# Kernel optimization log

Measured on AMD Instinct MI355X. Metric: run time of the kernel, lower is better.

## Reference

```python
import jax, jax.numpy as jnp
import numpy as np

EPS = 1e-5

def _lc(x, w, b, stride, pad):
    # x: [B,H,W]; w: [Ho,Wo,kh,kw]; b: [Ho,Wo]
    Ho, Wo, kh, kw = w.shape
    patches = jax.lax.conv_general_dilated_patches(
        x[:, None], (kh, kw), (stride, stride), [(pad, pad), (pad, pad)])
    # patches: [B, kh*kw, Ho, Wo]
    out = jnp.einsum('bkij,ijk->bij', patches, w.reshape(Ho, Wo, kh * kw))
    return out + b

def _ln2d(x, g, b):
    # torch LayerNorm over the last two (spatial) dims
    mu = x.mean(axis=(1, 2), keepdims=True)
    var = ((x - mu) ** 2).mean(axis=(1, 2), keepdims=True)
    return (x - mu) * jax.lax.rsqrt(var + EPS) * g + b

def _pool(x):
    # MaxPool2d(kernel=2, stride=2) over spatial dims of [B,H,W]
    return jax.lax.reduce_window(x, -jnp.inf, jax.lax.max, (1, 2, 2), (1, 2, 2), 'VALID')

def setup_inputs() -> dict:
    key = jax.random.key(0)
    ks = jax.random.split(key, 32)
    d = {}
    d['x'] = jax.random.normal(ks[0], (64, 128, 128), jnp.float32)
    sizes = [(128, 7), (64, 5), (64, 5), (32, 3), (32, 3), (16, 3)]
    for i, (s, k) in enumerate(sizes, start=1):
        d[f'w{i}'] = jax.random.normal(ks[4 * i], (s, s, k, k), jnp.float32) / k
        d[f'b{i}'] = jax.random.normal(ks[4 * i + 1], (s, s), jnp.float32)
        d[f'g{i}'] = jnp.ones((s, s), jnp.float32)
        d[f'be{i}'] = jnp.zeros((s, s), jnp.float32)
    d['fcw'] = jax.random.normal(ks[30], (1024, 256), jnp.float32) / np.sqrt(256.0)
    d['fcb'] = jax.random.normal(ks[31], (1024,), jnp.float32) * 0.01
    return d

def reference(x, w1, b1, g1, be1, w2, b2, g2, be2, w3, b3, g3, be3,
              w4, b4, g4, be4, w5, b5, g5, be5, w6, b6, g6, be6, fcw, fcb):
    # dropout is identity (eval / p=0)
    h = _pool(_ln2d(jax.nn.relu(_lc(x, w1, b1, 1, 3)), g1, be1))   # [B,64,64]
    h = _ln2d(jax.nn.relu(_lc(h, w2, b2, 1, 2)), g2, be2)          # [B,64,64]
    h = _pool(_ln2d(jax.nn.relu(_lc(h, w3, b3, 1, 2)), g3, be3))   # [B,32,32]
    h = _ln2d(jax.nn.relu(_lc(h, w4, b4, 1, 1)), g4, be4)          # [B,32,32]
    h = _pool(_ln2d(jax.nn.relu(_lc(h, w5, b5, 1, 1)), g5, be5))   # [B,16,16]
    h = _ln2d(jax.nn.relu(_lc(h, w6, b6, 1, 1)), g6, be6)          # [B,16,16]
    h = h.reshape(h.shape[0], -1) @ fcw.T + fcb                    # [B,1024]
    return jax.nn.softmax(h, axis=-1)
```

## Files before the change

### kernel.cpp

```cpp
#include <hip/hip_runtime.h>

#define LN_EPS 1e-5f

constexpr int T1_OFF   = 0;
constexpr int WT2_OFF  = 1048576;
constexpr int WT3_OFF  = WT2_OFF + 102400;
constexpr int WT4_OFF  = WT3_OFF + 102400;
constexpr int WT5_OFF  = WT4_OFF + 9216;
constexpr int WT6_OFF  = WT5_OFF + 9216;
constexpr int FCWT_OFF = WT6_OFF + 2304;
constexpr int R2_OFF   = FCWT_OFF + 262144;
constexpr int R3_OFF   = R2_OFF + 262144;
constexpr int R4_OFF   = R3_OFF + 262144;
constexpr int R5_OFF   = R4_OFF + 65536;
constexpr int ST1_OFF  = R5_OFF + 65536;
constexpr int ST2_OFF  = ST1_OFF + 32768;
constexpr int ST3_OFF  = ST2_OFF + 1024;
constexpr int ST4_OFF  = ST3_OFF + 1024;
constexpr int ST5_OFF  = ST4_OFF + 512;

constexpr int NREP = 136;

__global__ __launch_bounds__(256) void s1_conv(const float* __restrict__ x,
                                               const float* __restrict__ w1,
                                               const float* __restrict__ b1,
                                               const float* __restrict__ w2,
                                               const float* __restrict__ w3,
                                               const float* __restrict__ w4,
                                               const float* __restrict__ w5,
                                               const float* __restrict__ w6,
                                               const float* __restrict__ fcw,
                                               float* __restrict__ ws)
{
    const int tid = threadIdx.x;

    if (blockIdx.x < NREP) {
        const int rb = blockIdx.x;
        if (rb < 32) {
            for (int idx = rb * 256 + tid; idx < 102400; idx += 32 * 256) {
                int p = idx / 25, k = idx % 25;
                ws[WT2_OFF + k * 4096 + p] = w2[idx];
            }
        } else if (rb < 64) {
            for (int idx = (rb - 32) * 256 + tid; idx < 102400; idx += 32 * 256) {
                int p = idx / 25, k = idx % 25;
                ws[WT3_OFF + k * 4096 + p] = w3[idx];
            }
        } else if (rb < 68) {
            for (int idx = (rb - 64) * 256 + tid; idx < 9216; idx += 4 * 256) {
                int p = idx / 9, k = idx % 9;
                ws[WT4_OFF + k * 1024 + p] = w4[idx];
            }
        } else if (rb < 72) {
            for (int idx = (rb - 68) * 256 + tid; idx < 9216; idx += 4 * 256) {
                int p = idx / 9, k = idx % 9;
                ws[WT5_OFF + k * 1024 + p] = w5[idx];
            }
        } else if (rb < 73) {
            for (int idx = tid; idx < 2304; idx += 256) {
                int p = idx / 9, k = idx % 9;
                ws[WT6_OFF + k * 256 + p] = w6[idx];
            }
        } else {
            for (int idx = (rb - 73) * 256 + tid; idx < 262144; idx += 63 * 256) {
                int r = idx >> 8, kc = idx & 255;
                int kq = kc >> 2, c = kc & 3;
                ws[FCWT_OFF + kq * 4096 + r * 4 + c] = fcw[idx];
            }
        }
        return;
    }

    constexpr int R = 128, K = 7, TILE = 8, S = 16, PAD = 3;
    constexpr int RT = TILE + K - 1;
    constexpr int PP = RT * RT + 1;
    constexpr int NBLK = R / TILE;
    constexpr int WCNT = TILE * TILE * K * K;
    constexpr int PG = 256 / S;
    constexpr int OPT = TILE * TILE / PG;

    __shared__ float s_in[S * PP];
    __shared__ float s_w[WCNT];
    __shared__ float s_b[TILE * TILE];
    __shared__ float sp[4][16], sq[4][16];

    float* t1 = ws + T1_OFF;
    const int cb = blockIdx.x - NREP;
    const int bt = cb % (NBLK * NBLK);
    const int sg = cb / (NBLK * NBLK);
    const int i0 = (bt / NBLK) * TILE;
    const int j0 = (bt % NBLK) * TILE;
    const int S0 = sg * S;

    for (int idx = tid; idx < WCNT; idx += 256) {
        int pi = idx / (K * K), kk = idx % (K * K);
        int gi = i0 + pi / TILE, gj = j0 + pi % TILE;
        s_w[idx] = w1[(gi * R + gj) * (K * K) + kk];
    }
    if (tid < TILE * TILE)
        s_b[tid] = b1[(i0 + tid / TILE) * R + (j0 + tid % TILE)];

    for (int idx = tid; idx < S * RT * RT; idx += 256) {
        int ls = idx / (RT * RT), p = idx % (RT * RT);
        int ci = i0 - PAD + p / RT, cj = j0 - PAD + p % RT;
        float v = 0.0f;
        if (ci >= 0 && ci < R && cj >= 0 && cj < R)
            v = x[(S0 + ls) * R * R + ci * R + cj];
        s_in[ls * PP + p] = v;
    }
    __syncthreads();

    const int s = tid % S;
    const int pg = tid / S;
    const int p0 = pg * OPT;
    const int ti = p0 / TILE, tj0 = p0 % TILE;
    float acc[OPT];
    #pragma unroll
    for (int o = 0; o < OPT; o++) acc[o] = s_b[p0 + o];
    #pragma unroll
    for (int ki = 0; ki < K; ki++) {
        float row[OPT + K - 1];
        #pragma unroll
        for (int c = 0; c < OPT + K - 1; c++)
            row[c] = s_in[s * PP + (ti + ki) * RT + tj0 + c];
        #pragma unroll
        for (int kj = 0; kj < K; kj++)
            #pragma unroll
            for (int o = 0; o < OPT; o++)
                acc[o] += row[o + kj] * s_w[(p0 + o) * (K * K) + ki * K + kj];
    }
    float lsum = 0.f, lsq = 0.f;
    #pragma unroll
    for (int o = 0; o < OPT; o++) {
        float v = fmaxf(acc[o], 0.0f);
        t1[(S0 + s) * R * R + (i0 + ti) * R + (j0 + tj0 + o)] = v;
        lsum += v; lsq += v * v;
    }
    lsum += __shfl_xor(lsum, 16, 64); lsum += __shfl_xor(lsum, 32, 64);
    lsq  += __shfl_xor(lsq,  16, 64); lsq  += __shfl_xor(lsq,  32, 64);
    const int w = tid >> 6, l = tid & 63;
    if (l < 16) { sp[w][l] = lsum; sq[w][l] = lsq; }
    __syncthreads();
    if (tid < 16) {
        float a = sp[0][tid] + sp[1][tid] + sp[2][tid] + sp[3][tid];
        float b = sq[0][tid] + sq[1][tid] + sq[2][tid] + sq[3][tid];
        ws[ST1_OFF + (S0 + tid) * 512 + bt * 2]     = a;
        ws[ST1_OFF + (S0 + tid) * 512 + bt * 2 + 1] = b;
    }
}

__device__ __forceinline__ void block_sum2_256(float a, float b, float* red)
{
    const int tid = threadIdx.x;
    #pragma unroll
    for (int off = 32; off > 0; off >>= 1) {
        a += __shfl_down(a, off, 64);
        b += __shfl_down(b, off, 64);
    }
    if ((tid & 63) == 0) { red[tid >> 6] = a; red[4 + (tid >> 6)] = b; }
    __syncthreads();
    if (tid == 0) {
        red[0] = red[0] + red[1] + red[2] + red[3];
        red[4] = red[4] + red[5] + red[6] + red[7];
    }
    __syncthreads();
}

template<int M, int K, bool POOL>
__global__ __launch_bounds__(256) void stage_conv(
    const float* __restrict__ wsr, float* __restrict__ wsw,
    const float* __restrict__ g, const float* __restrict__ be,
    const float* __restrict__ bias,
    int inOff, int wtOff, int outOff,
    int stInOff, int nStatIn, float invNIn, int stOutOff)
{
    constexpr int NSLAB  = M / 8;
    constexpr int PADK   = (K - 1) / 2;
    constexpr int HR     = 8 + 2 * PADK;
    constexpr int IN_RES = POOL ? 2 * M : M;
    constexpr int STR    = M + 1;

    __shared__ float Isl[HR * STR];
    __shared__ float red[8];

    const int tid  = threadIdx.x;
    const int s    = blockIdx.x / NSLAB;
    const int slab = blockIdx.x % NSLAB;
    const int r0   = slab * 8;

    float a = 0.f, b = 0.f;
    for (int t = tid; t < nStatIn; t += 256) {
        a += wsr[stInOff + (s * nStatIn + t) * 2];
        b += wsr[stInOff + (s * nStatIn + t) * 2 + 1];
    }
    block_sum2_256(a, b, red);
    const float mu = red[0] * invNIn;
    const float rs = rsqrtf(red[4] * invNIn - mu * mu + LN_EPS);

    const float* In = wsr + inOff + s * (IN_RES * IN_RES);

    for (int idx = tid; idx < HR * M; idx += 256) {
        int lr = idx / M, jc = idx % M;
        int gr = r0 - PADK + lr;
        float v = 0.f;
        if (gr >= 0 && gr < M) {
            if constexpr (POOL) {
                float2 xa = *(const float2*)(In + (2 * gr) * IN_RES + 2 * jc);
                float2 xb = *(const float2*)(In + (2 * gr + 1) * IN_RES + 2 * jc);
                float2 ga = *(const float2*)(g  + (2 * gr) * IN_RES + 2 * jc);
                float2 gb = *(const float2*)(g  + (2 * gr + 1) * IN_RES + 2 * jc);
                float2 ea = *(const float2*)(be + (2 * gr) * IN_RES + 2 * jc);
                float2 eb = *(const float2*)(be + (2 * gr + 1) * IN_RES + 2 * jc);
                float n0 = (xa.x - mu) * rs * ga.x + ea.x;
                float n1 = (xa.y - mu) * rs * ga.y + ea.y;
                float n2 = (xb.x - mu) * rs * gb.x + eb.x;
                float n3 = (xb.y - mu) * rs * gb.y + eb.y;
                v = fmaxf(fmaxf(n0, n1), fmaxf(n2, n3));
            } else {
                int q = gr * M + jc;
                v = (In[q] - mu) * rs * g[q] + be[q];
            }
        }
        Isl[lr * STR + jc] = v;
    }
    __syncthreads();

    const float* wT = wsr + wtOff;
    constexpr int OPW = (8 * M) / 256;
    float lsum = 0.f, lsq = 0.f;
    #pragma unroll
    for (int o = 0; o < OPW; o++) {
        int p  = tid + o * 256;
        int li = p / M, j = p % M;
        int gi = r0 + li;
        int gp = gi * M + j;
        float acc = bias[gp];
        #pragma unroll
        for (int ki = 0; ki < K; ki++)
            #pragma unroll
            for (int kj = 0; kj < K; kj++) {
                int jj = j - PADK + kj;
                float iv = (jj >= 0 && jj < M) ? Isl[(li + ki) * STR + jj] : 0.f;
                acc += iv * wT[(ki * K + kj) * (M * M) + gp];
            }
        float v = fmaxf(acc, 0.f);
        wsw[outOff + s * (M * M) + gp] = v;
        lsum += v; lsq += v * v;
    }
    __syncthreads();
    block_sum2_256(lsum, lsq, red);
    if (tid == 0) {
        wsw[stOutOff + (s * NSLAB + slab) * 2]     = red[0];
        wsw[stOutOff + (s * NSLAB + slab) * 2 + 1] = red[4];
    }
}

constexpr int NT = 1024;
constexpr int NW = NT / 64;

__device__ __forceinline__ void stats_reduce(float* red, float lsum, float lsq,
                                             float inv_n, float* s_mu, float* s_rs)
{
    const int tid = threadIdx.x;
    #pragma unroll
    for (int off = 32; off > 0; off >>= 1) {
        lsum += __shfl_down(lsum, off, 64);
        lsq  += __shfl_down(lsq,  off, 64);
    }
    if ((tid & 63) == 0) { red[tid >> 6] = lsum; red[NW + (tid >> 6)] = lsq; }
    __syncthreads();
    if (tid == 0) {
        float a = 0.f, b = 0.f;
        #pragma unroll
        for (int i = 0; i < NW; i++) { a += red[i]; b += red[NW + i]; }
        float mu = a * inv_n, ms = b * inv_n;
        *s_mu = mu;
        *s_rs = rsqrtf(ms - mu * mu + LN_EPS);
    }
    __syncthreads();
}

__global__ __launch_bounds__(1024) void s6_tail(
    const float* __restrict__ wsr,
    const float* __restrict__ g5, const float* __restrict__ be5,
    const float* __restrict__ b6,
    const float* __restrict__ g6, const float* __restrict__ be6,
    const float* __restrict__ fcb,
    float* __restrict__ outp)
{
    __shared__ float I6[16 * 17];
    __shared__ float h[256];
    __shared__ float red[2 * NW];
    __shared__ float s_mu, s_rs;

    const int s = blockIdx.x;
    const int tid = threadIdx.x;

    if (tid == 0) {
        float a = 0.f, b = 0.f;
        #pragma unroll
        for (int i = 0; i < 4; i++) {
            a += wsr[ST5_OFF + (s * 4 + i) * 2];
            b += wsr[ST5_OFF + (s * 4 + i) * 2 + 1];
        }
        float mu = a * (1.f / 1024.f);
        s_mu = mu;
        s_rs = rsqrtf(b * (1.f / 1024.f) - mu * mu + LN_EPS);
    }
    __syncthreads();
    const float mu5 = s_mu, rs5 = s_rs;
    const float* R5 = wsr + R5_OFF + s * 1024;

    if (tid < 256) {
        int i = tid >> 4, j = tid & 15;
        float2 xa = *(const float2*)(R5 + (2 * i) * 32 + 2 * j);
        float2 xb = *(const float2*)(R5 + (2 * i + 1) * 32 + 2 * j);
        float2 ga = *(const float2*)(g5 + (2 * i) * 32 + 2 * j);
        float2 gb = *(const float2*)(g5 + (2 * i + 1) * 32 + 2 * j);
        float2 ea = *(const float2*)(be5 + (2 * i) * 32 + 2 * j);
        float2 eb = *(const float2*)(be5 + (2 * i + 1) * 32 + 2 * j);
        float n0 = (xa.x - mu5) * rs5 * ga.x + ea.x;
        float n1 = (xa.y - mu5) * rs5 * ga.y + ea.y;
        float n2 = (xb.x - mu5) * rs5 * gb.x + eb.x;
        float n3 = (xb.y - mu5) * rs5 * gb.y + eb.y;
        I6[i * 17 + j] = fmaxf(fmaxf(n0, n1), fmaxf(n2, n3));
    }
    __syncthreads();

    float v = 0.f, ls = 0.f, lq = 0.f;
    if (tid < 256) {
        int i = tid >> 4, j = tid & 15;
        const float* wT6 = wsr + WT6_OFF;
        float acc = b6[tid];
        #pragma unroll
        for (int ki = 0; ki < 3; ki++) {
            int ii = i - 1 + ki;
            bool rok = (ii >= 0 && ii < 16);
            #pragma unroll
            for (int kj = 0; kj < 3; kj++) {
                int jj = j - 1 + kj;
                float iv = (rok && jj >= 0 && jj < 16) ? I6[ii * 17 + jj] : 0.f;
                acc += iv * wT6[(ki * 3 + kj) * 256 + tid];
            }
        }
        v = fmaxf(acc, 0.f);
        ls = v; lq = v * v;
    }
    stats_reduce(red, ls, lq, 1.f / 256.f, &s_mu, &s_rs);
    if (tid < 256) h[tid] = (v - s_mu) * s_rs * g6[tid] + be6[tid];
    __syncthreads();

    float acc = fcb[tid];
    {
        const float4* wq = (const float4*)(wsr + FCWT_OFF);
        const float4* h4 = (const float4*)h;
        #pragma unroll 8
        for (int kq = 0; kq < 64; kq++) {
            float4 wv = wq[kq * 1024 + tid];
            float4 hv = h4[kq];
            acc += wv.x * hv.x + wv.y * hv.y + wv.z * hv.z + wv.w * hv.w;
        }
    }

    float m = acc;
    #pragma unroll
    for (int off = 32; off > 0; off >>= 1)
        m = fmaxf(m, __shfl_down(m, off, 64));
    if ((tid & 63) == 0) red[tid >> 6] = m;
    __syncthreads();
    if (tid == 0) {
        float mm = red[0];
        #pragma unroll
        for (int i = 1; i < NW; i++) mm = fmaxf(mm, red[i]);
        s_mu = mm;
    }
    __syncthreads();
    float e = expf(acc - s_mu);
    float sum = e;
    #pragma unroll
    for (int off = 32; off > 0; off >>= 1)
        sum += __shfl_down(sum, off, 64);
    if ((tid & 63) == 0) red[NW + (tid >> 6)] = sum;
    __syncthreads();
    if (tid == 0) {
        float ss = 0.f;
        #pragma unroll
        for (int i = 0; i < NW; i++) ss += red[NW + i];
        s_rs = 1.0f / ss;
    }
    __syncthreads();
    outp[s * 1024 + tid] = e * s_rs;
}

extern "C" void kernel_launch(void* const* d_in, const int* in_sizes, int n_in,
                              void* d_out, int out_size, void* d_ws, size_t ws_size,
                              hipStream_t stream) {
    (void)in_sizes; (void)n_in; (void)out_size; (void)ws_size;

    const float* x   = (const float*)d_in[0];
    const float* w1  = (const float*)d_in[1];  const float* b1  = (const float*)d_in[2];
    const float* g1  = (const float*)d_in[3];  const float* be1 = (const float*)d_in[4];
    const float* w2  = (const float*)d_in[5];  const float* b2  = (const float*)d_in[6];
    const float* g2  = (const float*)d_in[7];  const float* be2 = (const float*)d_in[8];
    const float* w3  = (const float*)d_in[9];  const float* b3  = (const float*)d_in[10];
    const float* g3  = (const float*)d_in[11]; const float* be3 = (const float*)d_in[12];
    const float* w4  = (const float*)d_in[13]; const float* b4  = (const float*)d_in[14];
    const float* g4  = (const float*)d_in[15]; const float* be4 = (const float*)d_in[16];
    const float* w5  = (const float*)d_in[17]; const float* b5  = (const float*)d_in[18];
    const float* g5  = (const float*)d_in[19]; const float* be5 = (const float*)d_in[20];
    const float* w6  = (const float*)d_in[21]; const float* b6  = (const float*)d_in[22];
    const float* g6  = (const float*)d_in[23]; const float* be6 = (const float*)d_in[24];
    const float* fcw = (const float*)d_in[25]; const float* fcb = (const float*)d_in[26];

    float* ws = (float*)d_ws;

    s1_conv<<<NREP + 1024, 256, 0, stream>>>(x, w1, b1, w2, w3, w4, w5, w6, fcw, ws);

    stage_conv<64, 5, true ><<<512, 256, 0, stream>>>(ws, ws, g1, be1, b2,
        T1_OFF, WT2_OFF, R2_OFF, ST1_OFF, 256, 1.f / 16384.f, ST2_OFF);
    stage_conv<64, 5, false><<<512, 256, 0, stream>>>(ws, ws, g2, be2, b3,
        R2_OFF, WT3_OFF, R3_OFF, ST2_OFF, 8, 1.f / 4096.f, ST3_OFF);
    stage_conv<32, 3, true ><<<256, 256, 0, stream>>>(ws, ws, g3, be3, b4,
        R3_OFF, WT4_OFF, R4_OFF, ST3_OFF, 8, 1.f / 4096.f, ST4_OFF);
    stage_conv<32, 3, false><<<256, 256, 0, stream>>>(ws, ws, g4, be4, b5,
        R4_OFF, WT5_OFF, R5_OFF, ST4_OFF, 4, 1.f / 1024.f, ST5_OFF);

    s6_tail<<<64, 1024, 0, stream>>>((const float*)ws,
        g5, be5, b6, g6, be6, fcb, (float*)d_out);
}
```

Before: 156.8 us.

## Fuse layers 4 and 5 into the tail kernel with per-sample shared-memory staging

```diff
diff --git a/kernel.cpp b/kernel.cpp
--- a/kernel.cpp
+++ b/kernel.cpp
@@ -11,13 +11,9 @@
 constexpr int FCWT_OFF = WT6_OFF + 2304;
 constexpr int R2_OFF   = FCWT_OFF + 262144;
 constexpr int R3_OFF   = R2_OFF + 262144;
-constexpr int R4_OFF   = R3_OFF + 262144;
-constexpr int R5_OFF   = R4_OFF + 65536;
-constexpr int ST1_OFF  = R5_OFF + 65536;
+constexpr int ST1_OFF  = R3_OFF + 262144;
 constexpr int ST2_OFF  = ST1_OFF + 32768;
 constexpr int ST3_OFF  = ST2_OFF + 1024;
-constexpr int ST4_OFF  = ST3_OFF + 1024;
-constexpr int ST5_OFF  = ST4_OFF + 512;
 
 constexpr int NREP = 136;
 
@@ -280,14 +276,20 @@
     __syncthreads();
 }
 
-__global__ __launch_bounds__(1024) void s6_tail(
+__global__ __launch_bounds__(1024) void tail46(
     const float* __restrict__ wsr,
+    const float* __restrict__ g3, const float* __restrict__ be3,
+    const float* __restrict__ b4,
+    const float* __restrict__ g4, const float* __restrict__ be4,
+    const float* __restrict__ b5,
     const float* __restrict__ g5, const float* __restrict__ be5,
     const float* __restrict__ b6,
     const float* __restrict__ g6, const float* __restrict__ be6,
     const float* __restrict__ fcb,
     float* __restrict__ outp)
 {
+    __shared__ float A[32 * 33];
+    __shared__ float B[32 * 33];
     __shared__ float I6[16 * 17];
     __shared__ float h[256];
     __shared__ float red[2 * NW];
@@ -295,59 +297,110 @@
 
     const int s = blockIdx.x;
     const int tid = threadIdx.x;
-
-    if (tid == 0) {
-        float a = 0.f, b = 0.f;
-        #pragma unroll
-        for (int i = 0; i < 4; i++) {
-            a += wsr[ST5_OFF + (s * 4 + i) * 2];
-            b += wsr[ST5_OFF + (s * 4 + i) * 2 + 1];
-        }
-        float mu = a * (1.f / 1024.f);
+    const int i = tid >> 5, j = tid & 31;
+
+    if (tid == 0) {
+        float a = 0.f, bq = 0.f;
+        #pragma unroll
+        for (int t = 0; t < 8; t++) {
+            a  += wsr[ST3_OFF + (s * 8 + t) * 2];
+            bq += wsr[ST3_OFF + (s * 8 + t) * 2 + 1];
+        }
+        float mu = a * (1.f / 4096.f);
         s_mu = mu;
-        s_rs = rsqrtf(b * (1.f / 1024.f) - mu * mu + LN_EPS);
-    }
-    __syncthreads();
-    const float mu5 = s_mu, rs5 = s_rs;
-    const float* R5 = wsr + R5_OFF + s * 1024;
-
-    if (tid < 256) {
-        int i = tid >> 4, j = tid & 15;
-        float2 xa = *(const float2*)(R5 + (2 * i) * 32 + 2 * j);
-        float2 xb = *(const float2*)(R5 + (2 * i + 1) * 32 + 2 * j);
-        float2 ga = *(const float2*)(g5 + (2 * i) * 32 + 2 * j);
-        float2 gb = *(const float2*)(g5 + (2 * i + 1) * 32 + 2 * j);
-        float2 ea = *(const float2*)(be5 + (2 * i) * 32 + 2 * j);
-        float2 eb = *(const float2*)(be5 + (2 * i + 1) * 32 + 2 * j);
-        float n0 = (xa.x - mu5) * rs5 * ga.x + ea.x;
-        float n1 = (xa.y - mu5) * rs5 * ga.y + ea.y;
-        float n2 = (xb.x - mu5) * rs5 * gb.x + eb.x;
-        float n3 = (xb.y - mu5) * rs5 * gb.y + eb.y;
-        I6[i * 17 + j] = fmaxf(fmaxf(n0, n1), fmaxf(n2, n3));
-    }
-    __syncthreads();
-
-    float v = 0.f, ls = 0.f, lq = 0.f;
-    if (tid < 256) {
-        int i = tid >> 4, j = tid & 15;
-        const float* wT6 = wsr + WT6_OFF;
-        float acc = b6[tid];
+        s_rs = rsqrtf(bq * (1.f / 4096.f) - mu * mu + LN_EPS);
+    }
+    __syncthreads();
+
+    {
+        const float mu = s_mu, rs = s_rs;
+        const float* R3 = wsr + R3_OFF + s * 4096;
+        float2 xa = *(const float2*)(R3  + (2 * i) * 64 + 2 * j);
+        float2 xb = *(const float2*)(R3  + (2 * i + 1) * 64 + 2 * j);
+        float2 ga = *(const float2*)(g3  + (2 * i) * 64 + 2 * j);
+        float2 gb = *(const float2*)(g3  + (2 * i + 1) * 64 + 2 * j);
+        float2 ea = *(const float2*)(be3 + (2 * i) * 64 + 2 * j);
+        float2 eb = *(const float2*)(be3 + (2 * i + 1) * 64 + 2 * j);
+        float n0 = (xa.x - mu) * rs * ga.x + ea.x;
+        float n1 = (xa.y - mu) * rs * ga.y + ea.y;
+        float n2 = (xb.x - mu) * rs * gb.x + eb.x;
+        float n3 = (xb.y - mu) * rs * gb.y + eb.y;
+        A[i * 33 + j] = fmaxf(fmaxf(n0, n1), fmaxf(n2, n3));
+    }
+    __syncthreads();
+
+    const float* wT4 = wsr + WT4_OFF;
+    const float* wT5 = wsr + WT5_OFF;
+    const float* wT6 = wsr + WT6_OFF;
+
+    float v4;
+    {
+        float acc = b4[tid];
         #pragma unroll
         for (int ki = 0; ki < 3; ki++) {
             int ii = i - 1 + ki;
-            bool rok = (ii >= 0 && ii < 16);
+            bool rok = (ii >= 0 && ii < 32);
             #pragma unroll
             for (int kj = 0; kj < 3; kj++) {
                 int jj = j - 1 + kj;
-                float iv = (rok && jj >= 0 && jj < 16) ? I6[ii * 17 + jj] : 0.f;
+                float iv = (rok && jj >= 0 && jj < 32) ? A[ii * 33 + jj] : 0.f;
+                acc += iv * wT4[(ki * 3 + kj) * 1024 + tid];
+            }
+        }
+        v4 = fmaxf(acc, 0.f);
+    }
+    stats_reduce(red, v4, v4 * v4, 1.f / 1024.f, &s_mu, &s_rs);
+    B[i * 33 + j] = (v4 - s_mu) * s_rs * g4[tid] + be4[tid];
+    __syncthreads();
+
+    float v5;
+    {
+        float acc = b5[tid];
+        #pragma unroll
+        for (int ki = 0; ki < 3; ki++) {
+            int ii = i - 1 + ki;
+            bool rok = (ii >= 0 && ii < 32);
+            #pragma unroll
+            for (int kj = 0; kj < 3; kj++) {
+                int jj = j - 1 + kj;
+                float iv = (rok && jj >= 0 && jj < 32) ? B[ii * 33 + jj] : 0.f;
+                acc += iv * wT5[(ki * 3 + kj) * 1024 + tid];
+            }
+        }
+        v5 = fmaxf(acc, 0.f);
+    }
+    stats_reduce(red, v5, v5 * v5, 1.f / 1024.f, &s_mu, &s_rs);
+    A[i * 33 + j] = (v5 - s_mu) * s_rs * g5[tid] + be5[tid];
+    __syncthreads();
+
+    if (tid < 256) {
+        int ii = tid >> 4, jj = tid & 15;
+        float p0 = A[(2 * ii) * 33 + 2 * jj],     p1 = A[(2 * ii) * 33 + 2 * jj + 1];
+        float p2 = A[(2 * ii + 1) * 33 + 2 * jj], p3 = A[(2 * ii + 1) * 33 + 2 * jj + 1];
+        I6[ii * 17 + jj] = fmaxf(fmaxf(p0, p1), fmaxf(p2, p3));
+    }
+    __syncthreads();
+
+    float v6 = 0.f, ls = 0.f, lq = 0.f;
+    if (tid < 256) {
+        int ii = tid >> 4, jj = tid & 15;
+        float acc = b6[tid];
+        #pragma unroll
+        for (int ki = 0; ki < 3; ki++) {
+            int ri = ii - 1 + ki;
+            bool rok = (ri >= 0 && ri < 16);
+            #pragma unroll
+            for (int kj = 0; kj < 3; kj++) {
+                int cj = jj - 1 + kj;
+                float iv = (rok && cj >= 0 && cj < 16) ? I6[ri * 17 + cj] : 0.f;
                 acc += iv * wT6[(ki * 3 + kj) * 256 + tid];
             }
         }
-        v = fmaxf(acc, 0.f);
-        ls = v; lq = v * v;
+        v6 = fmaxf(acc, 0.f);
+        ls = v6; lq = v6 * v6;
     }
     stats_reduce(red, ls, lq, 1.f / 256.f, &s_mu, &s_rs);
-    if (tid < 256) h[tid] = (v - s_mu) * s_rs * g6[tid] + be6[tid];
+    if (tid < 256) h[tid] = (v6 - s_mu) * s_rs * g6[tid] + be6[tid];
     __syncthreads();
 
     float acc = fcb[tid];
@@ -371,7 +424,7 @@
     if (tid == 0) {
         float mm = red[0];
         #pragma unroll
-        for (int i = 1; i < NW; i++) mm = fmaxf(mm, red[i]);
+        for (int t = 1; t < NW; t++) mm = fmaxf(mm, red[t]);
         s_mu = mm;
     }
     __syncthreads();
@@ -385,7 +438,7 @@
     if (tid == 0) {
         float ss = 0.f;
         #pragma unroll
-        for (int i = 0; i < NW; i++) ss += red[NW + i];
+        for (int t = 0; t < NW; t++) ss += red[NW + t];
         s_rs = 1.0f / ss;
     }
     __syncthreads();
@@ -420,11 +473,8 @@
         T1_OFF, WT2_OFF, R2_OFF, ST1_OFF, 256, 1.f / 16384.f, ST2_OFF);
     stage_conv<64, 5, false><<<512, 256, 0, stream>>>(ws, ws, g2, be2, b3,
         R2_OFF, WT3_OFF, R3_OFF, ST2_OFF, 8, 1.f / 4096.f, ST3_OFF);
-    stage_conv<32, 3, true ><<<256, 256, 0, stream>>>(ws, ws, g3, be3, b4,
-        R3_OFF, WT4_OFF, R4_OFF, ST3_OFF, 8, 1.f / 4096.f, ST4_OFF);
-    stage_conv<32, 3, false><<<256, 256, 0, stream>>>(ws, ws, g4, be4, b5,
-        R4_OFF, WT5_OFF, R5_OFF, ST4_OFF, 4, 1.f / 1024.f, ST5_OFF);
-
-    s6_tail<<<64, 1024, 0, stream>>>((const float*)ws,
-        g5, be5, b6, g6, be6, fcb, (float*)d_out);
-}
+
+    tail46<<<64, 1024, 0, stream>>>((const float*)ws,
+        g3, be3, b4, g4, be4, b5, g5, be5, b6, g6, be6,
+        fcb, (float*)d_out);
+}
```

Result: no change. 156.2 us (-0.4%).
